# Optimization experiments

Hardware: AMD Instinct MI355X
Metric: run time of the kernel (lower is better)

The kernel has to match this reference:

```python
import jax, jax.numpy as jnp
import numpy as np

E, D, H, T = 8, 2048, 5632, 32768  # experts, dim, hidden_dim, total routed tokens


def setup_inputs() -> dict:
    key = jax.random.key(0)
    k_x, k1, k2, k3 = jax.random.split(key, 4)
    x = jax.random.normal(k_x, (T, D), dtype=jnp.float32)
    # trunc_normal init stds per init_weights (approx: plain normal, same scale)
    std = (2.0 / (D * 24)) ** 0.5
    w1 = jax.random.normal(k1, (E, H, D), dtype=jnp.float32) * std
    w2 = jax.random.normal(k2, (E, D, H), dtype=jnp.float32) * std
    w3 = jax.random.normal(k3, (E, H, D), dtype=jnp.float32) * std
    # tokens are pre-sorted by expert; even split 4096 tokens/expert (sums to T)
    num_tokens_per_expert = jnp.full((E,), T // E, dtype=jnp.int32)
    return {"x": x, "w1": w1, "w2": w2, "w3": w3,
            "num_tokens_per_expert": num_tokens_per_expert}


def _grouped_experts(x, w1, w2, w3, counts):
    # Faithful to _run_experts_grouped_mm: grouped GEMMs computed in bf16,
    # SwiGLU activation, cast back to x dtype.
    xb = x.astype(jnp.bfloat16)
    w1b = jnp.transpose(w1.astype(jnp.bfloat16), (0, 2, 1))  # [E, D, H]
    w3b = jnp.transpose(w3.astype(jnp.bfloat16), (0, 2, 1))  # [E, D, H]
    w2b = jnp.transpose(w2.astype(jnp.bfloat16), (0, 2, 1))  # [E, H, D]
    h1 = jax.lax.ragged_dot(xb, w1b, counts)   # [T, H]
    h3 = jax.lax.ragged_dot(xb, w3b, counts)   # [T, H]
    h = jax.nn.silu(h1) * h3                   # fused SwiGLU gate
    out = jax.lax.ragged_dot(h, w2b, counts)   # [T, D]
    return out.astype(x.dtype)


def reference(x, w1, w2, w3, num_tokens_per_expert):
    return _grouped_experts(x, w1, w2, w3, num_tokens_per_expert)
```

## Files before the change

### kernel.cpp

```cpp
#include <hip/hip_runtime.h>
#include <hip/hip_bf16.h>
#include <stdint.h>

#define TT 32768
#define DD 2048
#define HH 5632
#define NE 8

typedef __bf16 bf16;
typedef __bf16 bf16x8 __attribute__((ext_vector_type(8)));
typedef float  f32x4  __attribute__((ext_vector_type(4)));

__device__ __forceinline__ void gl16(const void* g, void* l) {
    __builtin_amdgcn_global_load_lds(
        (const __attribute__((address_space(1))) void*)g,
        (__attribute__((address_space(3))) void*)l, 16, 0, 0);
}
#define VMW(n) asm volatile("s_waitcnt vmcnt(" #n ")" ::: "memory")
#define LGKM0() do { asm volatile("s_waitcnt lgkmcnt(0)" ::: "memory"); \
                     __builtin_amdgcn_sched_barrier(0); } while (0)
#define BARRIER() __builtin_amdgcn_s_barrier()

__device__ __forceinline__ int swz(int off) { return off ^ (((off >> 7) & 3) << 4); }

__device__ __forceinline__ int expert_of(const int* counts, int row0) {
    int base = 0;
    for (int i = 0; i < NE; ++i) { int c = counts[i]; if (row0 < base + c) return i; base += c; }
    return NE - 1;
}

__global__ __launch_bounds__(256)
void k_cvt(const float* __restrict__ in, bf16* __restrict__ out, long n) {
    long i = ((long)blockIdx.x * 256 + threadIdx.x) * 8;
    const long stride = (long)gridDim.x * 256 * 8;
    for (; i < n; i += stride) {
        const float4* p = (const float4*)(in + i);
        float4 a = p[0], b = p[1];
        union { bf16 v[8]; uint4 u; } r;
        r.v[0] = (bf16)a.x; r.v[1] = (bf16)a.y; r.v[2] = (bf16)a.z; r.v[3] = (bf16)a.w;
        r.v[4] = (bf16)b.x; r.v[5] = (bf16)b.y; r.v[6] = (bf16)b.z; r.v[7] = (bf16)b.w;
        *(uint4*)(out + i) = r.u;
    }
}

#define M1_LOAD(bufb, NA, NB1, NB3) do {                                      \
    const char* nb_ = sm + (bufb);                                            \
    _Pragma("unroll")                                                         \
    for (int mi = 0; mi < 8; ++mi)                                            \
        NA[mi] = *(const bf16x8*)(nb_ + aoff0 + mi * 1024);                   \
    _Pragma("unroll")                                                         \
    for (int ni = 0; ni < 2; ++ni) {                                          \
        NB1[ni] = *(const bf16x8*)(nb_ + 16384 + boff0 + ni * 1024);          \
        NB3[ni] = *(const bf16x8*)(nb_ + 24576 + boff0 + ni * 1024);          \
    }                                                                         \
    __builtin_amdgcn_sched_barrier(0);                                        \
} while (0)

#define M1_ITER(g, bLb, bSb, ko, CA, CB1, CB3, NA, NB1, NB3) do {             \
    if ((g) + 4 < GTOT) { stage((ko), (bSb)); VMW(8); }                       \
    else if ((g) == GTOT - 4) { VMW(4); }                                     \
    else if ((g) == GTOT - 3) { VMW(0); }                                     \
    LGKM0();                                                                  \
    if ((g) + 1 < GTOT) M1_LOAD((bLb), NA, NB1, NB3);                         \
    __builtin_amdgcn_s_setprio(1);                                            \
    _Pragma("unroll")                                                         \
    for (int mi = 0; mi < 8; ++mi)                                            \
    _Pragma("unroll")                                                         \
    for (int ni = 0; ni < 2; ++ni) {                                          \
        acc1[mi][ni] = __builtin_amdgcn_mfma_f32_16x16x32_bf16(CA[mi], CB1[ni], acc1[mi][ni], 0, 0, 0); \
        acc3[mi][ni] = __builtin_amdgcn_mfma_f32_16x16x32_bf16(CA[mi], CB3[ni], acc3[mi][ni], 0, 0, 0); \
    }                                                                         \
    __builtin_amdgcn_s_setprio(0);                                            \
    BARRIER();                                                                \
} while (0)

__global__ __launch_bounds__(512, 2)
void k_moe1(const bf16* __restrict__ xb, const bf16* __restrict__ w1b,
            const bf16* __restrict__ w3b, const int* __restrict__ counts,
            bf16* __restrict__ h) {
    extern __shared__ __align__(16) char sm[];
    const int tid = threadIdx.x;
    const int c = blockIdx.x & 7;
    const int j = blockIdx.x >> 3;
    const int NSEG = 22;
    const int NT = 64;
    const int GTOT = NSEG * NT;

    const int s0 = swz(tid * 16);
    const int s1 = 8192 + s0;
    const int dst0 = tid * 16;

    const char *sa0, *sa1, *sa2, *sa3;
    int sseg = 0;
    auto set_bases = [&](int sg) {
        int local = sg * 32 + j;
        int r0 = ((c << 4) + (local & 15)) * 256;
        int c0 = (local >> 4) * 128;
        int e = expert_of(counts, r0);
        sa0 = (const char*)xb + (((size_t)(r0 + (s0 >> 6)) * DD) << 1) + (s0 & 63);
        sa1 = (const char*)xb + (((size_t)(r0 + (s1 >> 6)) * DD) << 1) + (s1 & 63);
        const char* w1p = (const char*)(w1b + (size_t)e * HH * DD);
        const char* w3p = (const char*)(w3b + (size_t)e * HH * DD);
        sa2 = w1p + (((size_t)(c0 + (s0 >> 6)) * DD) << 1) + (s0 & 63);
        sa3 = w3p + (((size_t)(c0 + (s0 >> 6)) * DD) << 1) + (s0 & 63);
    };
    set_bases(0);

    auto stage = [&](int ko, int bufb) {
        char* db = sm + bufb;
        gl16(sa0 + ko, db + dst0);
        gl16(sa1 + ko, db + 8192 + dst0);
        gl16(sa2 + ko, db + 16384 + dst0);
        gl16(sa3 + ko, db + 24576 + dst0);
    };

    const int lane = tid & 63, wv = tid >> 6;
    const int wrow = wv >> 2, wcol = wv & 3;
    const int lrow = lane & 15, kb = (lane >> 4) << 4;
    const int aoff0 = swz((wrow * 128 + lrow) * 64 + kb);
    const int boff0 = swz((wcol * 32 + lrow) * 64 + kb);

    f32x4 acc1[8][2] = {};
    f32x4 acc3[8][2] = {};
    bf16x8 Xa[8], Xb1[2], Xb3[2], Ya[8], Yb1[2], Yb3[2];

    stage(0, 0); stage(64, 32768); stage(128, 65536); stage(192, 98304);
    VMW(8);
    BARRIER();
    M1_LOAD(0, Xa, Xb1, Xb3);

    int tc = 0, stk = 256, b0 = 0;
    int cseg = 0;
    int crow0 = ((c << 4) + (j & 15)) * 256;
    int ccol0 = (j >> 4) * 128;

    for (int gp = 0; gp < GTOT; gp += 2) {
        int bL1 = b0 + 1; if (bL1 >= 5) bL1 -= 5;
        int bL2 = b0 + 2; if (bL2 >= 5) bL2 -= 5;
        int bS1 = b0 + 4; if (bS1 >= 5) bS1 -= 5;
        const int bS2 = b0;
        if (tc == 60 && sseg + 1 < NSEG) { ++sseg; set_bases(sseg); stk = 0; }

        M1_ITER(gp,     bL1 << 15, bS1 << 15, stk,      Xa, Xb1, Xb3, Ya, Yb1, Yb3);
        M1_ITER(gp + 1, bL2 << 15, bS2 << 15, stk + 64, Ya, Yb1, Yb3, Xa, Xb1, Xb3);
        stk += 128;
        b0 += 2; if (b0 >= 5) b0 -= 5;

        if (tc == 62) {
#pragma unroll
            for (int mi = 0; mi < 8; ++mi)
#pragma unroll
                for (int ni = 0; ni < 2; ++ni) {
#pragma unroll
                    for (int jj = 0; jj < 4; ++jj) {
                        int row = crow0 + wrow * 128 + mi * 16 + ((lane >> 4) << 2) + jj;
                        int col = ccol0 + wcol * 32 + ni * 16 + lrow;
                        float f1 = (float)(bf16)acc1[mi][ni][jj];
                        float f3 = (float)(bf16)acc3[mi][ni][jj];
                        float s = f1 / (1.0f + __expf(-f1));
                        h[(size_t)row * HH + col] = (bf16)(s * f3);
                    }
                    acc1[mi][ni] = (f32x4){0.f, 0.f, 0.f, 0.f};
                    acc3[mi][ni] = (f32x4){0.f, 0.f, 0.f, 0.f};
                }
            ++cseg;
            int local = cseg * 32 + j;
            crow0 = ((c << 4) + (local & 15)) * 256;
            ccol0 = (local >> 4) * 128;
            tc = 0;
        } else {
            tc += 2;
        }
    }
}

#define G2_LOAD(t1, NA, NB) do {                                              \
    const char* nb_ = sm + (size_t)((t1) % 5) * 32768;                        \
    _Pragma("unroll")                                                         \
    for (int mi = 0; mi < 8; ++mi)                                            \
        NA[mi] = *(const bf16x8*)(nb_ + aoff0 + mi * 1024);                   \
    _Pragma("unroll")                                                         \
    for (int ni = 0; ni < 4; ++ni)                                            \
        NB[ni] = *(const bf16x8*)(nb_ + 16384 + boff0 + ni * 1024);           \
    __builtin_amdgcn_sched_barrier(0);                                        \
} while (0)

#define G2_ITER(t, CA, CB, NA, NB) do {                                       \
    if ((t) + 4 < NT) { stage((t) + 4); VMW(8); }                             \
    else if ((t) == NT - 4) { VMW(4); }                                       \
    else if ((t) == NT - 3) { VMW(0); }                                       \
    LGKM0();                                                                  \
    if ((t) + 1 < NT) G2_LOAD((t) + 1, NA, NB);                               \
    __builtin_amdgcn_s_setprio(1);                                            \
    _Pragma("unroll")                                                         \
    for (int mi = 0; mi < 8; ++mi)                                            \
    _Pragma("unroll")                                                         \
    for (int ni = 0; ni < 4; ++ni)                                            \
        acc[mi][ni] = __builtin_amdgcn_mfma_f32_16x16x32_bf16(CA[mi], CB[ni], acc[mi][ni], 0, 0, 0); \
    __builtin_amdgcn_s_setprio(0);                                            \
    BARRIER();                                                                \
} while (0)

__global__ __launch_bounds__(512, 2)
void k_g2(const bf16* __restrict__ hb, const bf16* __restrict__ w2b,
          const int* __restrict__ counts, float* __restrict__ out) {
    extern __shared__ __align__(16) char sm[];
    const int tid = threadIdx.x;
    const int c = blockIdx.x & 7;
    const int local = blockIdx.x >> 3;
    const int nt = local >> 4;
    const int mt = (c << 4) + (local & 15);
    const int row0 = mt * 256, col0 = nt * 256;
    const int e = expert_of(counts, row0);

    const char *sa0, *sa1, *sa2, *sa3;
    {
        int off0 = tid * 16, off1 = 8192 + tid * 16;
        int s0 = swz(off0), s1 = swz(off1);
        sa0 = (const char*)hb + (((size_t)(row0 + (s0 >> 6)) * HH) << 1) + (s0 & 63);
        sa1 = (const char*)hb + (((size_t)(row0 + (s1 >> 6)) * HH) << 1) + (s1 & 63);
        const char* wp = (const char*)(w2b + (size_t)e * DD * HH);
        sa2 = wp + (((size_t)(col0 + (s0 >> 6)) * HH) << 1) + (s0 & 63);
        sa3 = wp + (((size_t)(col0 + (s1 >> 6)) * HH) << 1) + (s1 & 63);
    }
    const int dst0 = tid * 16;
    auto stage = [&](int kt) {
        char* db = sm + (size_t)(kt % 5) * 32768;
        const size_t ko = (size_t)kt << 6;
        gl16(sa0 + ko, db + dst0);
        gl16(sa1 + ko, db + 8192 + dst0);
        gl16(sa2 + ko, db + 16384 + dst0);
        gl16(sa3 + ko, db + 24576 + dst0);
    };

    const int lane = tid & 63, wv = tid >> 6;
    const int wrow = wv >> 2, wcol = wv & 3;
    const int lrow = lane & 15, kb = (lane >> 4) << 4;

    const int aoff0 = swz((wrow * 128 + lrow) * 64 + kb);
    const int boff0 = swz((wcol * 64 + lrow) * 64 + kb);

    f32x4 acc[8][4] = {};
    bf16x8 Xa[8], Xb[4], Ya[8], Yb[4];

    const int NT = HH / 32;
    stage(0); stage(1); stage(2); stage(3);
    VMW(8);
    BARRIER();
    G2_LOAD(0, Xa, Xb);
    for (int t = 0; t < NT; t += 2) {
        G2_ITER(t,     Xa, Xb, Ya, Yb);
        G2_ITER(t + 1, Ya, Yb, Xa, Xb);
    }

#pragma unroll
    for (int mi = 0; mi < 8; ++mi)
#pragma unroll
        for (int ni = 0; ni < 4; ++ni)
#pragma unroll
            for (int j = 0; j < 4; ++j) {
                int row = row0 + wrow * 128 + mi * 16 + ((lane >> 4) << 2) + j;
                int col = col0 + wcol * 64 + ni * 16 + lrow;
                out[(size_t)row * DD + col] = (float)(bf16)acc[mi][ni][j];
            }
}

extern "C" void kernel_launch(void* const* d_in, const int* in_sizes, int n_in,
                              void* d_out, int out_size, void* d_ws, size_t ws_size,
                              hipStream_t stream) {
    const float* x      = (const float*)d_in[0];
    const float* w1     = (const float*)d_in[1];
    const float* w2     = (const float*)d_in[2];
    const float* w3     = (const float*)d_in[3];
    const int*   counts = (const int*)d_in[4];
    float* out = (float*)d_out;

    const size_t xb_b = (size_t)TT * DD * 2;
    const size_t h_b  = (size_t)TT * HH * 2;
    const size_t w_b  = (size_t)NE * HH * DD * 2;
    const size_t need_full = xb_b + h_b + 2 * w_b;
    if (ws_size < need_full) return;

    bf16* xb  = (bf16*)d_ws;
    bf16* h   = (bf16*)((char*)d_ws + xb_b);
    bf16* wsA = (bf16*)((char*)d_ws + xb_b + h_b);
    bf16* wsB = (bf16*)((char*)d_ws + xb_b + h_b + w_b);

    hipFuncSetAttribute((const void*)k_moe1, hipFuncAttributeMaxDynamicSharedMemorySize, 163840);
    hipFuncSetAttribute((const void*)k_g2,   hipFuncAttributeMaxDynamicSharedMemorySize, 163840);

    k_cvt<<<2048, 256, 0, stream>>>(x,  xb,  (long)TT * DD);
    k_cvt<<<2048, 256, 0, stream>>>(w1, wsA, (long)NE * HH * DD);
    k_cvt<<<2048, 256, 0, stream>>>(w3, wsB, (long)NE * HH * DD);
    k_moe1<<<256, 512, 163840, stream>>>(xb, wsA, wsB, counts, h);
    k_cvt<<<2048, 256, 0, stream>>>(w2, wsA, (long)NE * DD * HH);
    k_g2<<<1024, 512, 163840, stream>>>(h, wsA, counts, out);
}
```

Baseline: 2.648 ms.

## Halve GEMM tile sizes and use 256-thread blocks for both MoE kernels

Both grouped GEMM kernels move from 256-row tiles with 512-thread blocks to 128-row tiles with 256-thread blocks. Shared memory per block drops to 80KB and grid sizes grow, and k_moe1's persistent segment mapping now keeps a fixed row tile per block while stepping through column segments. The aim is more blocks resident per CU and better load balance. The cost is lower arithmetic intensity per tile, which means more global and LDS traffic per FLOP.

```diff
diff --git a/kernel.cpp b/kernel.cpp
--- a/kernel.cpp
+++ b/kernel.cpp
@@ -46,12 +46,12 @@
 #define M1_LOAD(bufb, NA, NB1, NB3) do {                                      \
     const char* nb_ = sm + (bufb);                                            \
     _Pragma("unroll")                                                         \
-    for (int mi = 0; mi < 8; ++mi)                                            \
+    for (int mi = 0; mi < 4; ++mi)                                            \
         NA[mi] = *(const bf16x8*)(nb_ + aoff0 + mi * 1024);                   \
     _Pragma("unroll")                                                         \
     for (int ni = 0; ni < 2; ++ni) {                                          \
-        NB1[ni] = *(const bf16x8*)(nb_ + 16384 + boff0 + ni * 1024);          \
-        NB3[ni] = *(const bf16x8*)(nb_ + 24576 + boff0 + ni * 1024);          \
+        NB1[ni] = *(const bf16x8*)(nb_ + 8192 + boff0 + ni * 1024);           \
+        NB3[ni] = *(const bf16x8*)(nb_ + 12288 + boff0 + ni * 1024);          \
     }                                                                         \
     __builtin_amdgcn_sched_barrier(0);                                        \
 } while (0)
@@ -64,7 +64,7 @@
     if ((g) + 1 < GTOT) M1_LOAD((bLb), NA, NB1, NB3);                         \
     __builtin_amdgcn_s_setprio(1);                                            \
     _Pragma("unroll")                                                         \
-    for (int mi = 0; mi < 8; ++mi)                                            \
+    for (int mi = 0; mi < 4; ++mi)                                            \
     _Pragma("unroll")                                                         \
     for (int ni = 0; ni < 2; ++ni) {                                          \
         acc1[mi][ni] = __builtin_amdgcn_mfma_f32_16x16x32_bf16(CA[mi], CB1[ni], acc1[mi][ni], 0, 0, 0); \
@@ -74,7 +74,7 @@
     BARRIER();                                                                \
 } while (0)
 
-__global__ __launch_bounds__(512, 2)
+__global__ __launch_bounds__(256, 2)
 void k_moe1(const bf16* __restrict__ xb, const bf16* __restrict__ w1b,
             const bf16* __restrict__ w3b, const int* __restrict__ counts,
             bf16* __restrict__ h) {
@@ -82,78 +82,78 @@
     const int tid = threadIdx.x;
     const int c = blockIdx.x & 7;
     const int j = blockIdx.x >> 3;
-    const int NSEG = 22;
+    const int NSEG = 44;
     const int NT = 64;
     const int GTOT = NSEG * NT;
 
+    const int mt = (c << 5) + (j & 31);
+    const int row0 = mt * 128;
+    const int e = expert_of(counts, row0);
+
     const int s0 = swz(tid * 16);
-    const int s1 = 8192 + s0;
+    const int s1 = 4096 + s0;
     const int dst0 = tid * 16;
 
-    const char *sa0, *sa1, *sa2, *sa3;
+    const char* sa0 = (const char*)xb + (((size_t)(row0 + (s0 >> 6)) * DD) << 1) + (s0 & 63);
+    const char* sa1 = (const char*)xb + (((size_t)(row0 + (s1 >> 6)) * DD) << 1) + (s1 & 63);
+    const char* w1p = (const char*)(w1b + (size_t)e * HH * DD);
+    const char* w3p = (const char*)(w3b + (size_t)e * HH * DD);
+    const char *sa2, *sa3;
     int sseg = 0;
-    auto set_bases = [&](int sg) {
-        int local = sg * 32 + j;
-        int r0 = ((c << 4) + (local & 15)) * 256;
-        int c0 = (local >> 4) * 128;
-        int e = expert_of(counts, r0);
-        sa0 = (const char*)xb + (((size_t)(r0 + (s0 >> 6)) * DD) << 1) + (s0 & 63);
-        sa1 = (const char*)xb + (((size_t)(r0 + (s1 >> 6)) * DD) << 1) + (s1 & 63);
-        const char* w1p = (const char*)(w1b + (size_t)e * HH * DD);
-        const char* w3p = (const char*)(w3b + (size_t)e * HH * DD);
+    auto set_b = [&](int sg) {
+        int c0 = (sg * 2 + (j >> 5)) * 64;
         sa2 = w1p + (((size_t)(c0 + (s0 >> 6)) * DD) << 1) + (s0 & 63);
         sa3 = w3p + (((size_t)(c0 + (s0 >> 6)) * DD) << 1) + (s0 & 63);
     };
-    set_bases(0);
+    set_b(0);
 
     auto stage = [&](int ko, int bufb) {
         char* db = sm + bufb;
         gl16(sa0 + ko, db + dst0);
-        gl16(sa1 + ko, db + 8192 + dst0);
-        gl16(sa2 + ko, db + 16384 + dst0);
-        gl16(sa3 + ko, db + 24576 + dst0);
+        gl16(sa1 + ko, db + 4096 + dst0);
+        gl16(sa2 + ko, db + 8192 + dst0);
+        gl16(sa3 + ko, db + 12288 + dst0);
     };
 
     const int lane = tid & 63, wv = tid >> 6;
-    const int wrow = wv >> 2, wcol = wv & 3;
+    const int wrow = wv >> 1, wcol = wv & 1;
     const int lrow = lane & 15, kb = (lane >> 4) << 4;
-    const int aoff0 = swz((wrow * 128 + lrow) * 64 + kb);
+    const int aoff0 = swz((wrow * 64 + lrow) * 64 + kb);
     const int boff0 = swz((wcol * 32 + lrow) * 64 + kb);
 
-    f32x4 acc1[8][2] = {};
-    f32x4 acc3[8][2] = {};
-    bf16x8 Xa[8], Xb1[2], Xb3[2], Ya[8], Yb1[2], Yb3[2];
-
-    stage(0, 0); stage(64, 32768); stage(128, 65536); stage(192, 98304);
+    f32x4 acc1[4][2] = {};
+    f32x4 acc3[4][2] = {};
+    bf16x8 Xa[4], Xb1[2], Xb3[2], Ya[4], Yb1[2], Yb3[2];
+
+    stage(0, 0); stage(64, 16384); stage(128, 32768); stage(192, 49152);
     VMW(8);
     BARRIER();
     M1_LOAD(0, Xa, Xb1, Xb3);
 
     int tc = 0, stk = 256, b0 = 0;
     int cseg = 0;
-    int crow0 = ((c << 4) + (j & 15)) * 256;
-    int ccol0 = (j >> 4) * 128;
+    int ccol0 = (j >> 5) * 64;
 
     for (int gp = 0; gp < GTOT; gp += 2) {
         int bL1 = b0 + 1; if (bL1 >= 5) bL1 -= 5;
         int bL2 = b0 + 2; if (bL2 >= 5) bL2 -= 5;
         int bS1 = b0 + 4; if (bS1 >= 5) bS1 -= 5;
         const int bS2 = b0;
-        if (tc == 60 && sseg + 1 < NSEG) { ++sseg; set_bases(sseg); stk = 0; }
-
-        M1_ITER(gp,     bL1 << 15, bS1 << 15, stk,      Xa, Xb1, Xb3, Ya, Yb1, Yb3);
-        M1_ITER(gp + 1, bL2 << 15, bS2 << 15, stk + 64, Ya, Yb1, Yb3, Xa, Xb1, Xb3);
+        if (tc == 60 && sseg + 1 < NSEG) { ++sseg; set_b(sseg); stk = 0; }
+
+        M1_ITER(gp,     bL1 << 14, bS1 << 14, stk,      Xa, Xb1, Xb3, Ya, Yb1, Yb3);
+        M1_ITER(gp + 1, bL2 << 14, bS2 << 14, stk + 64, Ya, Yb1, Yb3, Xa, Xb1, Xb3);
         stk += 128;
         b0 += 2; if (b0 >= 5) b0 -= 5;
 
         if (tc == 62) {
 #pragma unroll
-            for (int mi = 0; mi < 8; ++mi)
+            for (int mi = 0; mi < 4; ++mi)
 #pragma unroll
                 for (int ni = 0; ni < 2; ++ni) {
 #pragma unroll
                     for (int jj = 0; jj < 4; ++jj) {
-                        int row = crow0 + wrow * 128 + mi * 16 + ((lane >> 4) << 2) + jj;
+                        int row = row0 + wrow * 64 + mi * 16 + ((lane >> 4) << 2) + jj;
                         int col = ccol0 + wcol * 32 + ni * 16 + lrow;
                         float f1 = (float)(bf16)acc1[mi][ni][jj];
                         float f3 = (float)(bf16)acc3[mi][ni][jj];
@@ -164,9 +164,7 @@
                     acc3[mi][ni] = (f32x4){0.f, 0.f, 0.f, 0.f};
                 }
             ++cseg;
-            int local = cseg * 32 + j;
-            crow0 = ((c << 4) + (local & 15)) * 256;
-            ccol0 = (local >> 4) * 128;
+            ccol0 = (cseg * 2 + (j >> 5)) * 64;
             tc = 0;
         } else {
             tc += 2;
@@ -175,13 +173,13 @@
 }
 
 #define G2_LOAD(t1, NA, NB) do {                                              \
-    const char* nb_ = sm + (size_t)((t1) % 5) * 32768;                        \
-    _Pragma("unroll")                                                         \
-    for (int mi = 0; mi < 8; ++mi)                                            \
+    const char* nb_ = sm + (size_t)((t1) % 5) * 16384;                        \
+    _Pragma("unroll")                                                         \
+    for (int mi = 0; mi < 4; ++mi)                                            \
         NA[mi] = *(const bf16x8*)(nb_ + aoff0 + mi * 1024);                   \
     _Pragma("unroll")                                                         \
     for (int ni = 0; ni < 4; ++ni)                                            \
-        NB[ni] = *(const bf16x8*)(nb_ + 16384 + boff0 + ni * 1024);           \
+        NB[ni] = *(const bf16x8*)(nb_ + 8192 + boff0 + ni * 1024);            \
     __builtin_amdgcn_sched_barrier(0);                                        \
 } while (0)
 
@@ -193,7 +191,7 @@
     if ((t) + 1 < NT) G2_LOAD((t) + 1, NA, NB);                               \
     __builtin_amdgcn_s_setprio(1);                                            \
     _Pragma("unroll")                                                         \
-    for (int mi = 0; mi < 8; ++mi)                                            \
+    for (int mi = 0; mi < 4; ++mi)                                            \
     _Pragma("unroll")                                                         \
     for (int ni = 0; ni < 4; ++ni)                                            \
         acc[mi][ni] = __builtin_amdgcn_mfma_f32_16x16x32_bf16(CA[mi], CB[ni], acc[mi][ni], 0, 0, 0); \
@@ -201,47 +199,45 @@
     BARRIER();                                                                \
 } while (0)
 
-__global__ __launch_bounds__(512, 2)
+__global__ __launch_bounds__(256, 2)
 void k_g2(const bf16* __restrict__ hb, const bf16* __restrict__ w2b,
           const int* __restrict__ counts, float* __restrict__ out) {
     extern __shared__ __align__(16) char sm[];
     const int tid = threadIdx.x;
     const int c = blockIdx.x & 7;
     const int local = blockIdx.x >> 3;
-    const int nt = local >> 4;
-    const int mt = (c << 4) + (local & 15);
-    const int row0 = mt * 256, col0 = nt * 256;
+    const int mt = (c << 5) + (local & 31);
+    const int nt = local >> 5;
+    const int row0 = mt * 128, col0 = nt * 128;
     const int e = expert_of(counts, row0);
 
-    const char *sa0, *sa1, *sa2, *sa3;
-    {
-        int off0 = tid * 16, off1 = 8192 + tid * 16;
-        int s0 = swz(off0), s1 = swz(off1);
-        sa0 = (const char*)hb + (((size_t)(row0 + (s0 >> 6)) * HH) << 1) + (s0 & 63);
-        sa1 = (const char*)hb + (((size_t)(row0 + (s1 >> 6)) * HH) << 1) + (s1 & 63);
-        const char* wp = (const char*)(w2b + (size_t)e * DD * HH);
-        sa2 = wp + (((size_t)(col0 + (s0 >> 6)) * HH) << 1) + (s0 & 63);
-        sa3 = wp + (((size_t)(col0 + (s1 >> 6)) * HH) << 1) + (s1 & 63);
-    }
+    const int s0 = swz(tid * 16);
+    const int s1 = 4096 + s0;
     const int dst0 = tid * 16;
+
+    const char* sa0 = (const char*)hb + (((size_t)(row0 + (s0 >> 6)) * HH) << 1) + (s0 & 63);
+    const char* sa1 = (const char*)hb + (((size_t)(row0 + (s1 >> 6)) * HH) << 1) + (s1 & 63);
+    const char* wp = (const char*)(w2b + (size_t)e * DD * HH);
+    const char* sa2 = wp + (((size_t)(col0 + (s0 >> 6)) * HH) << 1) + (s0 & 63);
+    const char* sa3 = wp + (((size_t)(col0 + (s1 >> 6)) * HH) << 1) + (s1 & 63);
+
     auto stage = [&](int kt) {
-        char* db = sm + (size_t)(kt % 5) * 32768;
+        char* db = sm + (size_t)(kt % 5) * 16384;
         const size_t ko = (size_t)kt << 6;
         gl16(sa0 + ko, db + dst0);
-        gl16(sa1 + ko, db + 8192 + dst0);
-        gl16(sa2 + ko, db + 16384 + dst0);
-        gl16(sa3 + ko, db + 24576 + dst0);
+        gl16(sa1 + ko, db + 4096 + dst0);
+        gl16(sa2 + ko, db + 8192 + dst0);
+        gl16(sa3 + ko, db + 12288 + dst0);
     };
 
     const int lane = tid & 63, wv = tid >> 6;
-    const int wrow = wv >> 2, wcol = wv & 3;
+    const int wrow = wv >> 1, wcol = wv & 1;
     const int lrow = lane & 15, kb = (lane >> 4) << 4;
-
-    const int aoff0 = swz((wrow * 128 + lrow) * 64 + kb);
+    const int aoff0 = swz((wrow * 64 + lrow) * 64 + kb);
     const int boff0 = swz((wcol * 64 + lrow) * 64 + kb);
 
-    f32x4 acc[8][4] = {};
-    bf16x8 Xa[8], Xb[4], Ya[8], Yb[4];
+    f32x4 acc[4][4] = {};
+    bf16x8 Xa[4], Xb[4], Ya[4], Yb[4];
 
     const int NT = HH / 32;
     stage(0); stage(1); stage(2); stage(3);
@@ -254,12 +250,12 @@
     }
 
 #pragma unroll
-    for (int mi = 0; mi < 8; ++mi)
+    for (int mi = 0; mi < 4; ++mi)
 #pragma unroll
         for (int ni = 0; ni < 4; ++ni)
 #pragma unroll
             for (int j = 0; j < 4; ++j) {
-                int row = row0 + wrow * 128 + mi * 16 + ((lane >> 4) << 2) + j;
+                int row = row0 + wrow * 64 + mi * 16 + ((lane >> 4) << 2) + j;
                 int col = col0 + wcol * 64 + ni * 16 + lrow;
                 out[(size_t)row * DD + col] = (float)(bf16)acc[mi][ni][j];
             }
@@ -286,13 +282,13 @@
     bf16* wsA = (bf16*)((char*)d_ws + xb_b + h_b);
     bf16* wsB = (bf16*)((char*)d_ws + xb_b + h_b + w_b);
 
-    hipFuncSetAttribute((const void*)k_moe1, hipFuncAttributeMaxDynamicSharedMemorySize, 163840);
-    hipFuncSetAttribute((const void*)k_g2,   hipFuncAttributeMaxDynamicSharedMemorySize, 163840);
+    hipFuncSetAttribute((const void*)k_moe1, hipFuncAttributeMaxDynamicSharedMemorySize, 81920);
+    hipFuncSetAttribute((const void*)k_g2,   hipFuncAttributeMaxDynamicSharedMemorySize, 81920);
 
     k_cvt<<<2048, 256, 0, stream>>>(x,  xb,  (long)TT * DD);
     k_cvt<<<2048, 256, 0, stream>>>(w1, wsA, (long)NE * HH * DD);
     k_cvt<<<2048, 256, 0, stream>>>(w3, wsB, (long)NE * HH * DD);
-    k_moe1<<<256, 512, 163840, stream>>>(xb, wsA, wsB, counts, h);
+    k_moe1<<<512, 256, 81920, stream>>>(xb, wsA, wsB, counts, h);
     k_cvt<<<2048, 256, 0, stream>>>(w2, wsA, (long)NE * DD * HH);
-    k_g2<<<1024, 512, 163840, stream>>>(h, wsA, counts, out);
-}
+    k_g2<<<4096, 256, 81920, stream>>>(h, wsA, counts, out);
+}
```

New measurement: 3.943 ms. 48.9% more time.
